# Performance work log

Measured on AMD Instinct MI355X. Metric: run time of the kernel, lower is better.

Reference implementation:

```python
import jax, jax.numpy as jnp
import numpy as np

BETA = 0.25
NUM_EMBEDS = 1024
EMBED_DIM = 256


def setup_inputs() -> dict:
    key = jax.random.key(0)
    k1, k2 = jax.random.split(key)
    z_e = jax.random.normal(k1, (32, EMBED_DIM, 1024), dtype=jnp.float32)
    lim = 1.0 / NUM_EMBEDS
    embed_weight = jax.random.uniform(k2, (NUM_EMBEDS, EMBED_DIM), dtype=jnp.float32,
                                      minval=-lim, maxval=lim)
    return {"z_e": z_e, "embed_weight": embed_weight}


def reference(z_e, embed_weight):
    # z_e: (b, d, t) -> (b, t, d)
    ze = jnp.transpose(z_e, (0, 2, 1))
    b, t, d = ze.shape
    flat = ze.reshape(-1, d)  # (N, d)
    K = embed_weight.shape[0]
    # squared euclidean distances (N, K) via sum-of-squares + matmul
    distances = (jnp.sum(flat ** 2, axis=1, keepdims=True)
                 + jnp.sum(embed_weight ** 2, axis=1)
                 - 2.0 * flat @ embed_weight.T)
    idx = jnp.argmin(distances, axis=1)  # (N,)
    # one-hot @ W is just a gather
    z_q = embed_weight[idx].reshape(b, t, d)
    # commitment / codebook losses (mse over all elements)
    e_latent_loss = jnp.mean((jax.lax.stop_gradient(z_q) - ze) ** 2)
    q_latent_loss = jnp.mean((z_q - jax.lax.stop_gradient(ze)) ** 2)
    reg_loss = q_latent_loss + BETA * e_latent_loss
    # straight-through estimator
    z_q_st = ze + jax.lax.stop_gradient(z_q - ze)
    z_q_out = jnp.transpose(z_q_st, (0, 2, 1))  # (b, d, t)
    # perplexity from codebook usage
    N = flat.shape[0]
    avg_probs = jnp.zeros((K,), dtype=jnp.float32).at[idx].add(1.0) / N
    perplexity = jnp.exp(-jnp.sum(avg_probs * jnp.log(avg_probs + 1e-10)))
    return (z_q_out, reg_loss, perplexity)
```

## Files before the change

kernel.cpp:

```cpp
#include <hip/hip_runtime.h>
#include <math.h>

#define BB 32
#define DD 256
#define TT 1024
#define KK 1024
#define NN (BB*TT)

#define BROWS 64
#define CCH   256
#define WSL   32
#define NSTEP 32


__global__ void prep_kernel(const float* __restrict__ W, float* __restrict__ wsq,
                            int* __restrict__ counts, float* __restrict__ sse) {
    const int k = blockIdx.x;
    const int lane = threadIdx.x;
    const float4 v = ((const float4*)(W + (size_t)k * DD))[lane];
    double s = (double)v.x * v.x + (double)v.y * v.y + (double)v.z * v.z + (double)v.w * v.w;
    #pragma unroll
    for (int m = 32; m > 0; m >>= 1) s += __shfl_down(s, m);
    if (lane == 0) wsq[k] = (float)s;
    if (blockIdx.x < 16) counts[blockIdx.x * 64 + lane] = 0;
    if (blockIdx.x == 0 && lane == 0) *sse = 0.0f;
}

__device__ __forceinline__ int swz_z(int r, int q) { return r * 16 + (q ^ (r & 7) ^ ((r >> 3) & 7)); }
__device__ __forceinline__ int swz_w(int r, int q) { return r * 8 + (q ^ ((r >> 3) & 7)); }

__device__ __forceinline__ void gl_lds16(const float* g, void* l) {
    __builtin_amdgcn_global_load_lds((const __attribute__((address_space(1))) void*)g,
                                     (__attribute__((address_space(3))) void*)l, 16, 0, 0);
}

__global__ __launch_bounds__(256, 2) void vq_fused_kernel(
    const float* __restrict__ z, const float* __restrict__ W,
    const float* __restrict__ wsq, float* __restrict__ out,
    int* __restrict__ counts, float* __restrict__ sse)
{
    __shared__ float4 zs[BROWS * 16];
    __shared__ float4 ws[2][CCH * 8];
    const int tid = threadIdx.x;
    const int tx = tid & 31, ty = tid >> 5;
    const int w = tid >> 6, lane = tid & 63;
    const int row0 = blockIdx.x * BROWS;
    const int b = row0 >> 10, t0 = row0 & 1023;
    const size_t bbase = (size_t)b * DD * TT;
    const float* zbase = z + bbase + t0;

    const int zr  = lane;
    const int zq0 = w * 4;
    const int wlr = lane >> 3;
    const int wls = lane & 7;
    float4 zreg[4];

    {
        const float* wch = W;
        char* dst = (char*)&ws[0][0] + (size_t)w * 8192;
        #pragma unroll
        for (int k = 0; k < 8; ++k) {
            const int r = w * 64 + k * 8 + wlr;
            gl_lds16(wch + (size_t)r * DD + 4 * (wls ^ k), dst + k * 1024);
        }
        #pragma unroll
        for (int j = 0; j < 4; ++j) {
            const float* zp = zbase + (size_t)((zq0 + j) * 4) * TT + zr;
            zreg[j].x = zp[0]; zreg[j].y = zp[(size_t)TT];
            zreg[j].z = zp[(size_t)2 * TT]; zreg[j].w = zp[(size_t)3 * TT];
        }
    }

    float rsq[8];
    {
        const int ro = lane & 15;
        const int g  = lane >> 4;
        const float* zp = zbase + (size_t)g * 64 * TT + (16 * w + ro);
        double s = 0.0;
        #pragma unroll 4
        for (int d = 0; d < 64; ++d) { float v = zp[(size_t)d * TT]; s += (double)v * v; }
        s += __shfl_xor(s, 16);
        s += __shfl_xor(s, 32);
        float f = (float)s;
        #pragma unroll
        for (int i = 0; i < 8; ++i) rsq[i] = __shfl(f, (ty & 1) * 8 + i);
    }

    float minv[8]; int mini[8];
    #pragma unroll
    for (int i = 0; i < 8; ++i) { minv[i] = 3.4e38f; mini[i] = 0; }

    float acc[8][8];
    float wq[8];

    for (int s = 0; s < NSTEP; ++s) {
        const int h = s & 1, sl = s & 7, ch = s >> 3;
        __syncthreads();
        if (h == 0) {
            #pragma unroll
            for (int j = 0; j < 4; ++j) zs[swz_z(zr, zq0 + j)] = zreg[j];
            __syncthreads();
        }
        if (s + 1 < NSTEP) {
            const int t = s + 1, sln = t & 7, chn = t >> 3;
            const float* wch = W + (size_t)(chn * CCH) * DD + sln * WSL;
            char* dst = (char*)&ws[t & 1][0] + (size_t)w * 8192;
            #pragma unroll
            for (int k = 0; k < 8; ++k) {
                const int r = w * 64 + k * 8 + wlr;
                gl_lds16(wch + (size_t)r * DD + 4 * (wls ^ k), dst + k * 1024);
            }
        }
        if (h == 0 && s + 2 < NSTEP) {
            const int mn = ((s + 2) & 7) >> 1;
            #pragma unroll
            for (int j = 0; j < 4; ++j) {
                const float* zp = zbase + (size_t)(mn * 64 + (zq0 + j) * 4) * TT + zr;
                zreg[j].x = zp[0]; zreg[j].y = zp[(size_t)TT];
                zreg[j].z = zp[(size_t)2 * TT]; zreg[j].w = zp[(size_t)3 * TT];
            }
        }
        if (sl == 0) {
            #pragma unroll
            for (int i = 0; i < 8; ++i)
                #pragma unroll
                for (int j = 0; j < 8; ++j) acc[i][j] = 0.0f;
            #pragma unroll
            for (int j = 0; j < 8; ++j) wq[j] = wsq[ch * CCH + tx * 8 + j];
        }
        const int qb = 8 * h;
        for (int q = 0; q < 8; ++q) {
            float4 zf[8], wf[8];
            #pragma unroll
            for (int i = 0; i < 8; ++i) zf[i] = zs[swz_z(ty * 8 + i, qb + q)];
            #pragma unroll
            for (int j = 0; j < 8; ++j) wf[j] = ws[h][swz_w(tx * 8 + j, q)];
            #pragma unroll
            for (int i = 0; i < 8; ++i)
                #pragma unroll
                for (int j = 0; j < 8; ++j) {
                    acc[i][j] = fmaf(zf[i].x, wf[j].x, acc[i][j]);
                    acc[i][j] = fmaf(zf[i].y, wf[j].y, acc[i][j]);
                    acc[i][j] = fmaf(zf[i].z, wf[j].z, acc[i][j]);
                    acc[i][j] = fmaf(zf[i].w, wf[j].w, acc[i][j]);
                }
        }
        if (sl == 7) {
            #pragma unroll
            for (int j = 0; j < 8; ++j) {
                int c = ch * CCH + tx * 8 + j;
                #pragma unroll
                for (int i = 0; i < 8; ++i) {
                    float s1 = rsq[i] + wq[j];
                    float v = fmaf(-2.0f, acc[i][j], s1);
                    if (v < minv[i]) { minv[i] = v; mini[i] = c; }
                }
            }
        }
    }

    __syncthreads();
    int* idxs = (int*)&zs[0];
    float* ssescr = (float*)&zs[0] + 64;
    #pragma unroll
    for (int i = 0; i < 8; ++i) {
        float v = minv[i]; int ix = mini[i];
        #pragma unroll
        for (int m = 1; m < 32; m <<= 1) {
            float ov = __shfl_xor(v, m);
            int   oi = __shfl_xor(ix, m);
            if (ov < v || (ov == v && oi < ix)) { v = ov; ix = oi; }
        }
        if (tx == 0) {
            idxs[ty * 8 + i] = ix;
            atomicAdd(&counts[ix], 1);
        }
    }
    __syncthreads();

    const int tg = tid & 15;
    const int dg = tid >> 4;
    const int t4 = tg * 4;
    int ixs[4];
    #pragma unroll
    for (int m = 0; m < 4; ++m) ixs[m] = idxs[t4 + m];
    float ssel = 0.0f;
    #pragma unroll
    for (int k4 = 0; k4 < 4; ++k4) {
        const int d0 = dg * 16 + k4 * 4;
        float wr[4][4];
        #pragma unroll
        for (int m = 0; m < 4; ++m) {
            float4 wv = *(const float4*)(W + (size_t)ixs[m] * DD + d0);
            wr[m][0] = wv.x; wr[m][1] = wv.y; wr[m][2] = wv.z; wr[m][3] = wv.w;
        }
        #pragma unroll
        for (int dd = 0; dd < 4; ++dd) {
            const int d = d0 + dd;
            const size_t base = bbase + (size_t)d * TT + t0 + t4;
            float4 zv = *(const float4*)(z + base);
            float e0 = wr[0][dd] - zv.x, e1 = wr[1][dd] - zv.y;
            float e2 = wr[2][dd] - zv.z, e3 = wr[3][dd] - zv.w;
            float4 o;
            o.x = zv.x + e0; o.y = zv.y + e1; o.z = zv.z + e2; o.w = zv.w + e3;
            *(float4*)(out + base) = o;
            ssel += (e0 * e0 + e1 * e1) + (e2 * e2 + e3 * e3);
        }
    }
    #pragma unroll
    for (int m = 32; m > 0; m >>= 1) ssel += __shfl_down(ssel, m);
    if (lane == 0) ssescr[w] = ssel;
    __syncthreads();
    if (tid == 0) atomicAdd(sse, (ssescr[0] + ssescr[1]) + (ssescr[2] + ssescr[3]));
}

__global__ void finalize_kernel(const int* __restrict__ counts, const float* __restrict__ sse,
                                float* __restrict__ out) {
    float s = 0.0f;
    for (int k = threadIdx.x; k < KK; k += 256) {
        float p = (float)counts[k] / (float)NN;
        s += p * logf(p + 1e-10f);
    }
    #pragma unroll
    for (int m = 32; m > 0; m >>= 1) s += __shfl_down(s, m);
    __shared__ float wsum[4];
    if ((threadIdx.x & 63) == 0) wsum[threadIdx.x >> 6] = s;
    __syncthreads();
    if (threadIdx.x == 0) {
        float ent = (wsum[0] + wsum[1]) + (wsum[2] + wsum[3]);
        out[(size_t)BB * DD * TT]     = 1.25f * (*sse) / (float)(BB * DD * TT);
        out[(size_t)BB * DD * TT + 1] = expf(-ent);
    }
}

extern "C" void kernel_launch(void* const* d_in, const int* in_sizes, int n_in,
                              void* d_out, int out_size, void* d_ws, size_t ws_size,
                              hipStream_t stream) {
    const float* z = (const float*)d_in[0];
    const float* W = (const float*)d_in[1];
    float* out = (float*)d_out;

    float* wsq    = (float*)d_ws;
    int*   counts = (int*)(wsq + 1024);
    float* sse    = (float*)(counts + 1024);

    prep_kernel<<<1024, 64, 0, stream>>>(W, wsq, counts, sse);
    vq_fused_kernel<<<NN / BROWS, 256, 0, stream>>>(z, W, wsq, out, counts, sse);
    finalize_kernel<<<1, 256, 0, stream>>>(counts, sse, out);
}
```

Baseline: 278.6 us.

## Double row tile to 128 with 16x8 register tile and per-step z staging

```diff
diff --git a/kernel.cpp b/kernel.cpp
--- a/kernel.cpp
+++ b/kernel.cpp
@@ -7,9 +7,8 @@
 #define KK 1024
 #define NN (BB*TT)
 
-#define BROWS 64
+#define BROWS 128
 #define CCH   256
-#define WSL   32
 #define NSTEP 32
 
 
@@ -26,131 +25,127 @@
     if (blockIdx.x == 0 && lane == 0) *sse = 0.0f;
 }
 
-__device__ __forceinline__ int swz_z(int r, int q) { return r * 16 + (q ^ (r & 7) ^ ((r >> 3) & 7)); }
-__device__ __forceinline__ int swz_w(int r, int q) { return r * 8 + (q ^ ((r >> 3) & 7)); }
-
 __device__ __forceinline__ void gl_lds16(const float* g, void* l) {
     __builtin_amdgcn_global_load_lds((const __attribute__((address_space(1))) void*)g,
                                      (__attribute__((address_space(3))) void*)l, 16, 0, 0);
 }
 
-__global__ __launch_bounds__(256, 2) void vq_fused_kernel(
+__global__ __launch_bounds__(256, 1) void vq_fused_kernel(
     const float* __restrict__ z, const float* __restrict__ W,
     const float* __restrict__ wsq, float* __restrict__ out,
     int* __restrict__ counts, float* __restrict__ sse)
 {
-    __shared__ float4 zs[BROWS * 16];
+    __shared__ float4 zst[8][BROWS];
     __shared__ float4 ws[2][CCH * 8];
     const int tid = threadIdx.x;
     const int tx = tid & 31, ty = tid >> 5;
     const int w = tid >> 6, lane = tid & 63;
+    const int txc = tx & 7;
+    const int zr = tid & 127, hh = tid >> 7;
     const int row0 = blockIdx.x * BROWS;
     const int b = row0 >> 10, t0 = row0 & 1023;
     const size_t bbase = (size_t)b * DD * TT;
     const float* zbase = z + bbase + t0;
 
-    const int zr  = lane;
-    const int zq0 = w * 4;
-    const int wlr = lane >> 3;
-    const int wls = lane & 7;
     float4 zreg[4];
 
     {
-        const float* wch = W;
         char* dst = (char*)&ws[0][0] + (size_t)w * 8192;
         #pragma unroll
         for (int k = 0; k < 8; ++k) {
-            const int r = w * 64 + k * 8 + wlr;
-            gl_lds16(wch + (size_t)r * DD + 4 * (wls ^ k), dst + k * 1024);
+            const int r = w * 64 + k * 8 + (lane >> 3);
+            gl_lds16(W + (size_t)r * DD + 4 * ((lane & 7) ^ k), dst + k * 1024);
         }
         #pragma unroll
         for (int j = 0; j < 4; ++j) {
-            const float* zp = zbase + (size_t)((zq0 + j) * 4) * TT + zr;
+            const float* zp = zbase + (size_t)((hh * 4 + j) * 4) * TT + zr;
             zreg[j].x = zp[0]; zreg[j].y = zp[(size_t)TT];
             zreg[j].z = zp[(size_t)2 * TT]; zreg[j].w = zp[(size_t)3 * TT];
         }
     }
 
-    float rsq[8];
+    float rsq[16];
     {
-        const int ro = lane & 15;
-        const int g  = lane >> 4;
-        const float* zp = zbase + (size_t)g * 64 * TT + (16 * w + ro);
-        double s = 0.0;
+        double* pscr = (double*)&zst[0][0];
+        float*  fscr = (float*)&zst[4][0];
+        const float* zp = zbase + (size_t)(2 * hh) * 64 * TT + zr;
+        double sA = 0.0, sB = 0.0;
         #pragma unroll 4
-        for (int d = 0; d < 64; ++d) { float v = zp[(size_t)d * TT]; s += (double)v * v; }
-        s += __shfl_xor(s, 16);
-        s += __shfl_xor(s, 32);
-        float f = (float)s;
-        #pragma unroll
-        for (int i = 0; i < 8; ++i) rsq[i] = __shfl(f, (ty & 1) * 8 + i);
-    }
-
-    float minv[8]; int mini[8];
-    #pragma unroll
-    for (int i = 0; i < 8; ++i) { minv[i] = 3.4e38f; mini[i] = 0; }
-
-    float acc[8][8];
+        for (int d = 0; d < 64; ++d) { float v = zp[(size_t)d * TT]; sA += (double)v * v; }
+        const float* zp2 = zp + (size_t)64 * TT;
+        #pragma unroll 4
+        for (int d = 0; d < 64; ++d) { float v = zp2[(size_t)d * TT]; sB += (double)v * v; }
+        pscr[hh * 128 + zr] = sA + sB;
+        __syncthreads();
+        if (tid < 128) fscr[tid] = (float)(pscr[tid] + pscr[128 + tid]);
+        __syncthreads();
+        #pragma unroll
+        for (int i = 0; i < 16; ++i) rsq[i] = fscr[ty * 16 + i];
+    }
+
+    float minv[16]; int mini[16];
+    #pragma unroll
+    for (int i = 0; i < 16; ++i) { minv[i] = 3.4e38f; mini[i] = 0; }
+
+    float acc[16][8];
     float wq[8];
 
-    for (int s = 0; s < NSTEP; ++s) {
-        const int h = s & 1, sl = s & 7, ch = s >> 3;
-        __syncthreads();
-        if (h == 0) {
-            #pragma unroll
-            for (int j = 0; j < 4; ++j) zs[swz_z(zr, zq0 + j)] = zreg[j];
-            __syncthreads();
-        }
-        if (s + 1 < NSTEP) {
-            const int t = s + 1, sln = t & 7, chn = t >> 3;
-            const float* wch = W + (size_t)(chn * CCH) * DD + sln * WSL;
-            char* dst = (char*)&ws[t & 1][0] + (size_t)w * 8192;
+    for (int t = 0; t < NSTEP; ++t) {
+        const int sl = t & 7, ch = t >> 3, h = t & 1;
+        __syncthreads();
+        #pragma unroll
+        for (int j = 0; j < 4; ++j) zst[hh * 4 + j][zr] = zreg[j];
+        __syncthreads();
+        asm volatile("s_waitcnt vmcnt(0)" ::: "memory");
+        if (t + 1 < NSTEP) {
+            const int tn = t + 1, chn = tn >> 3, sln = tn & 7;
+            const float* wch = W + (size_t)(chn * CCH) * DD + sln * 32;
+            char* dst = (char*)&ws[tn & 1][0] + (size_t)w * 8192;
             #pragma unroll
             for (int k = 0; k < 8; ++k) {
-                const int r = w * 64 + k * 8 + wlr;
-                gl_lds16(wch + (size_t)r * DD + 4 * (wls ^ k), dst + k * 1024);
-            }
-        }
-        if (h == 0 && s + 2 < NSTEP) {
-            const int mn = ((s + 2) & 7) >> 1;
+                const int r = w * 64 + k * 8 + (lane >> 3);
+                gl_lds16(wch + (size_t)r * DD + 4 * ((lane & 7) ^ k), dst + k * 1024);
+            }
             #pragma unroll
             for (int j = 0; j < 4; ++j) {
-                const float* zp = zbase + (size_t)(mn * 64 + (zq0 + j) * 4) * TT + zr;
+                const float* zp = zbase + (size_t)(sln * 32 + (hh * 4 + j) * 4) * TT + zr;
                 zreg[j].x = zp[0]; zreg[j].y = zp[(size_t)TT];
                 zreg[j].z = zp[(size_t)2 * TT]; zreg[j].w = zp[(size_t)3 * TT];
             }
         }
         if (sl == 0) {
             #pragma unroll
-            for (int i = 0; i < 8; ++i)
+            for (int i = 0; i < 16; ++i)
                 #pragma unroll
                 for (int j = 0; j < 8; ++j) acc[i][j] = 0.0f;
             #pragma unroll
             for (int j = 0; j < 8; ++j) wq[j] = wsq[ch * CCH + tx * 8 + j];
         }
-        const int qb = 8 * h;
+        const float4* wb0 = &ws[h][tx * 64];
+        #pragma clang loop unroll(disable)
         for (int q = 0; q < 8; ++q) {
-            float4 zf[8], wf[8];
-            #pragma unroll
-            for (int i = 0; i < 8; ++i) zf[i] = zs[swz_z(ty * 8 + i, qb + q)];
-            #pragma unroll
-            for (int j = 0; j < 8; ++j) wf[j] = ws[h][swz_w(tx * 8 + j, q)];
-            #pragma unroll
-            for (int i = 0; i < 8; ++i)
+            const float4* wp = wb0 + (q ^ txc);
+            float4 wf[8];
+            #pragma unroll
+            for (int j = 0; j < 8; ++j) wf[j] = wp[j * 8];
+            #pragma unroll
+            for (int i = 0; i < 16; ++i) {
+                float4 z4 = zst[q][ty * 16 + i];
                 #pragma unroll
                 for (int j = 0; j < 8; ++j) {
-                    acc[i][j] = fmaf(zf[i].x, wf[j].x, acc[i][j]);
-                    acc[i][j] = fmaf(zf[i].y, wf[j].y, acc[i][j]);
-                    acc[i][j] = fmaf(zf[i].z, wf[j].z, acc[i][j]);
-                    acc[i][j] = fmaf(zf[i].w, wf[j].w, acc[i][j]);
+                    acc[i][j] = fmaf(z4.x, wf[j].x, acc[i][j]);
+                    acc[i][j] = fmaf(z4.y, wf[j].y, acc[i][j]);
+                    acc[i][j] = fmaf(z4.z, wf[j].z, acc[i][j]);
+                    acc[i][j] = fmaf(z4.w, wf[j].w, acc[i][j]);
                 }
+            }
         }
         if (sl == 7) {
             #pragma unroll
             for (int j = 0; j < 8; ++j) {
-                int c = ch * CCH + tx * 8 + j;
+                const int c = ch * CCH + tx * 8 + j;
                 #pragma unroll
-                for (int i = 0; i < 8; ++i) {
+                for (int i = 0; i < 16; ++i) {
                     float s1 = rsq[i] + wq[j];
                     float v = fmaf(-2.0f, acc[i][j], s1);
                     if (v < minv[i]) { minv[i] = v; mini[i] = c; }
@@ -160,10 +155,10 @@
     }
 
     __syncthreads();
-    int* idxs = (int*)&zs[0];
-    float* ssescr = (float*)&zs[0] + 64;
-    #pragma unroll
-    for (int i = 0; i < 8; ++i) {
+    int* idxs = (int*)&zst[0][0];
+    float* ssescr = (float*)&zst[0][0] + 256;
+    #pragma unroll
+    for (int i = 0; i < 16; ++i) {
         float v = minv[i]; int ix = mini[i];
         #pragma unroll
         for (int m = 1; m < 32; m <<= 1) {
@@ -172,22 +167,22 @@
             if (ov < v || (ov == v && oi < ix)) { v = ov; ix = oi; }
         }
         if (tx == 0) {
-            idxs[ty * 8 + i] = ix;
+            idxs[ty * 16 + i] = ix;
             atomicAdd(&counts[ix], 1);
         }
     }
     __syncthreads();
 
-    const int tg = tid & 15;
-    const int dg = tid >> 4;
+    const int tg = tid & 31;
+    const int dg = tid >> 5;
     const int t4 = tg * 4;
     int ixs[4];
     #pragma unroll
     for (int m = 0; m < 4; ++m) ixs[m] = idxs[t4 + m];
     float ssel = 0.0f;
     #pragma unroll
-    for (int k4 = 0; k4 < 4; ++k4) {
-        const int d0 = dg * 16 + k4 * 4;
+    for (int k4 = 0; k4 < 8; ++k4) {
+        const int d0 = dg * 32 + k4 * 4;
         float wr[4][4];
         #pragma unroll
         for (int m = 0; m < 4; ++m) {
```

Measured after the change: 306.9 us. 10.1% more time.
